# Performance work log

Hardware: AMD Instinct MI355X
Metric: run time of the kernel (lower is better)

## Reference

```python
import jax, jax.numpy as jnp
import numpy as np
from jax import lax

B, T, D, H = 4, 4096, 1024, 8
DK, DV = 1024, 2048          # expand_k=1.0, expand_v=2.0
RANK, MAXL, LOOPD = 16, 8, 128  # lora_rank, max_loops, dim*loop_dim_fraction
THRESH = 0.99
EPS = 1e-6
GK_SCALE = 16.0              # GLA forget-gate temperature


def setup_inputs() -> dict:
    key = jax.random.key(0)
    ks = jax.random.split(key, 16)
    r = lambda i, shape, s=0.02: jax.random.normal(ks[i], shape, jnp.float32) * s
    return {
        "h": jax.random.normal(ks[0], (B, T, D), jnp.float32),
        "e": jax.random.normal(ks[1], (B, T, D), jnp.float32),
        "norm_w": jnp.ones((D,), jnp.float32),
        "out_norm_w": jnp.ones((D,), jnp.float32),
        "Wq": r(2, (D, DK)), "Wk": r(3, (D, DK)), "Wv": r(4, (D, DV)),
        "Wgk": r(5, (D, DK)), "Wg": r(6, (D, DV)), "Wo": r(7, (DV, D)),
        "lora_A": r(8, (MAXL, D, RANK)), "lora_B": r(9, (MAXL, RANK, D)),
        "inj_A": 0.9 * jnp.eye(D, dtype=jnp.float32) + r(10, (D, D)),
        "inj_B": r(11, (D, D)),
        "act_w": r(12, (D,)),
        "act_b": jnp.full((), -2.0, jnp.float32),  # gradual halting
        "loop_table": r(13, (MAXL, LOOPD)),
        "n_loops": 4,
    }


def rmsnorm(x, w):
    return x * lax.rsqrt(jnp.mean(x * x, axis=-1, keepdims=True) + EPS) * w


def gla(x, Wq, Wk, Wv, Wgk, Wg, Wo, num_heads):
    """Gated Linear Attention: data-dependent forget gates, linear-time recurrent scan."""
    b, t, d = x.shape
    dk, dv = Wq.shape[1], Wv.shape[1]
    dkh, dvh = dk // num_heads, dv // num_heads
    q = (x @ Wq).reshape(b, t, num_heads, dkh) * (dkh ** -0.5)
    k = (x @ Wk).reshape(b, t, num_heads, dkh)
    v = (x @ Wv).reshape(b, t, num_heads, dvh)
    # forget gate alpha in (0,1): exp(logsigmoid(gk)/16)
    alpha = jnp.exp(jax.nn.log_sigmoid(x @ Wgk) / GK_SCALE).reshape(b, t, num_heads, dkh)

    def step(S, qkva):  # S: (b, H, dkh, dvh)
        qt, kt, vt, at = qkva
        S = at[..., None] * S + kt[..., None] * vt[..., None, :]
        ot = jnp.einsum('bhk,bhkv->bhv', qt, S)
        return S, ot

    S0 = jnp.zeros((b, num_heads, dkh, dvh), x.dtype)
    xs = (jnp.swapaxes(q, 0, 1), jnp.swapaxes(k, 0, 1),
          jnp.swapaxes(v, 0, 1), jnp.swapaxes(alpha, 0, 1))
    _, o = lax.scan(step, S0, xs)                  # o: (t, b, H, dvh)
    o = jnp.swapaxes(o, 0, 1).reshape(b, t, dv)
    o = o * jax.nn.silu(x @ Wg)                    # output gate
    return o @ Wo


def reference(h, e, norm_w, out_norm_w, Wq, Wk, Wv, Wgk, Wg, Wo,
              lora_A, lora_B, inj_A, inj_B, act_w, act_b, loop_table, n_loops):
    b, t_len, d = h.shape
    halted = jnp.zeros((b, t_len), bool)
    cum = jnp.zeros((b, t_len), h.dtype)
    h_out = jnp.zeros_like(h)
    loopd = loop_table.shape[1]
    for t in range(n_loops):  # small fixed depth loop (structurally distinct LoRA/embed per t)
        # loop index embedding on first loopd channels
        h = h.at[..., :loopd].add(loop_table[t])
        h_norm = rmsnorm(h + e, norm_w)
        g = gla(h_norm, Wq, Wk, Wv, Wgk, Wg, Wo, H)   # dropout: eval mode (identity)
        g = g + (g @ lora_A[t]) @ lora_B[t]            # depth LoRA
        h = h @ inj_A.T + e @ inj_B.T + g              # LTI injection: A.h + B.e + gla
        # ACT halting accumulate
        p = jax.nn.sigmoid(h @ act_w + act_b)          # (b, t_len)
        running = ~halted
        p_eff = jnp.where(running, p, jnp.zeros_like(p))
        new_cum = cum + p_eff
        newly = running & (new_cum >= THRESH)
        w = jnp.where(newly, 1.0 - cum, p_eff)         # remainder for newly-halted
        h_out = h_out + w[..., None] * h
        cum = new_cum
        halted = halted | newly
    return rmsnorm(h_out, out_norm_w)
```

## Files before the change

### kernel.cpp

```cpp
#include <hip/hip_runtime.h>

#define BB 4
#define TT 4096
#define DD 1024
#define HH 8
#define DKK 1024
#define DVV 2048
#define MR (BB*TT)
#define DKH 128
#define DVH 256
#define NLOOPS 4
#define LCH 128
#define NCH (TT/LCH)
#define PADW 136
#define NPROJ 7168

#define WS_NEED 662310912ull

__device__ __attribute__((aligned(256))) unsigned char g_ws[WS_NEED];

typedef __bf16 bf16x8 __attribute__((ext_vector_type(8)));
typedef float  f32x4  __attribute__((ext_vector_type(4)));

__device__ __forceinline__ unsigned short f2bfu(float f) {
    unsigned int u = __builtin_bit_cast(unsigned int, f);
    u += 0x7fffu + ((u >> 16) & 1u);
    return (unsigned short)(u >> 16);
}
__device__ __forceinline__ float bfu2f(unsigned short s) {
    unsigned int u = ((unsigned int)s) << 16;
    return __builtin_bit_cast(float, u);
}

__device__ __forceinline__ void gld_lds16(const void* g, void* l) {
    __builtin_amdgcn_global_load_lds(
        (__attribute__((address_space(1))) void*)const_cast<void*>(g),
        (__attribute__((address_space(3))) void*)l, 16, 0, 0);
}

__global__ __launch_bounds__(256) void k_transpose_bf16(
    const float* __restrict__ in, unsigned short* __restrict__ out, int K, int N)
{
    __shared__ float tile[64][65];
    int k0 = blockIdx.y * 64, n0 = blockIdx.x * 64;
    int tx = threadIdx.x & 63, ty = threadIdx.x >> 6;
    #pragma unroll
    for (int r = 0; r < 64; r += 4)
        tile[ty + r][tx] = in[(size_t)(k0 + ty + r) * N + n0 + tx];
    __syncthreads();
    #pragma unroll
    for (int r = 0; r < 64; r += 4)
        out[(size_t)(n0 + ty + r) * K + k0 + tx] = f2bfu(tile[tx][ty + r]);
}

__global__ __launch_bounds__(256) void k_conv_e(
    const float* __restrict__ e, unsigned short* __restrict__ he)
{
    size_t gid = (size_t)blockIdx.x * 256 + threadIdx.x;
    size_t b4 = gid * 4;
    size_t row = b4 >> 10; int col = (int)(b4 & 1023);
    float4 v = *(const float4*)&e[row * 1024 + col];
    *(ushort4*)&he[row * 2048 + 1024 + col] =
        make_ushort4(f2bfu(v.x), f2bfu(v.y), f2bfu(v.z), f2bfu(v.w));
}

__global__ __launch_bounds__(256) void k_conv_injcomb(
    const float* __restrict__ injA, const float* __restrict__ injB,
    unsigned short* __restrict__ WinjT, float* __restrict__ diag)
{
    int idx = blockIdx.x * 256 + threadIdx.x;
    int i = idx >> 10, j = idx & 1023;
    float va = injA[idx], vb = injB[idx];
    unsigned short ua;
    if (i == j) { diag[i] = va; ua = 0; }
    else        { ua = f2bfu(va); }
    WinjT[(size_t)i * 2048 + j] = ua;
    WinjT[(size_t)i * 2048 + 1024 + j] = f2bfu(vb);
}

__global__ __launch_bounds__(256) void k_prep(
    float* __restrict__ h, const float* __restrict__ e,
    const float* __restrict__ norm_w, const float* __restrict__ ltab,
    unsigned short* __restrict__ he, unsigned short* __restrict__ xn_bf)
{
    int row = blockIdx.x, tid = threadIdx.x;
    size_t base = (size_t)row * DD + tid * 4;
    float4 hv = *(float4*)&h[base];
    if (tid < 32) {
        float4 lv = *(const float4*)&ltab[tid * 4];
        hv.x += lv.x; hv.y += lv.y; hv.z += lv.z; hv.w += lv.w;
        *(float4*)&h[base] = hv;
    }
    float4 ev = *(const float4*)&e[base];
    float sx = hv.x + ev.x, sy = hv.y + ev.y, sz = hv.z + ev.z, sw = hv.w + ev.w;
    float partial = sx*sx + sy*sy + sz*sz + sw*sw;
    __shared__ float red[256];
    red[tid] = partial; __syncthreads();
    for (int st = 128; st > 0; st >>= 1) {
        if (tid < st) red[tid] += red[tid + st];
        __syncthreads();
    }
    float rms = rsqrtf(red[0] * (1.0f / DD) + 1e-6f);
    float4 wv = *(const float4*)&norm_w[tid * 4];
    *(ushort4*)&xn_bf[base] = make_ushort4(
        f2bfu(sx * rms * wv.x), f2bfu(sy * rms * wv.y),
        f2bfu(sz * rms * wv.z), f2bfu(sw * rms * wv.w));
    *(ushort4*)&he[(size_t)row * 2048 + tid * 4] =
        make_ushort4(f2bfu(hv.x), f2bfu(hv.y), f2bfu(hv.z), f2bfu(hv.w));
}

template<int KB>
__device__ __forceinline__ void gemm8_core(
    const char* __restrict__ Ab, const char* __restrict__ Bb,
    int bm, int bn, char* sm, f32x4 (&acc)[8][4])
{
    constexpr int NKT = KB / 128;
    const int tid = threadIdx.x;
    const int lane = tid & 63;
    const int wave = tid >> 6;
    const int wm = wave >> 2, wn = wave & 3;
    const int ln15 = lane & 15, q4 = lane >> 4;
    const int xorv = (ln15 & 7) << 4;
    const int xc0 = (q4 * 16) ^ xorv;
    const int xc1 = (64 + q4 * 16) ^ xorv;

    const int L0 = tid * 16;
    const int L1 = 8192 + tid * 16;
    const int lin0 = L0 ^ (((L0 >> 7) & 7) << 4);
    const int lin1 = L1 ^ (((L1 >> 7) & 7) << 4);
    const int sr0 = lin0 >> 7, sc0 = lin0 & 127;
    const int sr1 = lin1 >> 7, sc1 = lin1 & 127;

    bf16x8 av[4][2];
    bf16x8 bv[2][2][2];

    auto STAGE = [&](const char* gb, int row0, int kcol, int region) {
        gld_lds16(gb + (size_t)(row0 + sr0) * KB + (kcol + sc0), sm + region + L0);
        gld_lds16(gb + (size_t)(row0 + sr1) * KB + (kcol + sc1), sm + region + L1);
    };

#define LD_AV(CB, MH) \
    _Pragma("unroll") \
    for (int i2 = 0; i2 < 4; ++i2) { \
        const char* rp = sm + (CB) + ((MH) * 16384) \
                       + ((wm * 64 + i2 * 16 + ln15) * 128); \
        av[i2][0] = *(const bf16x8*)(rp + xc0); \
        av[i2][1] = *(const bf16x8*)(rp + xc1); \
    }
#define LD_BV(CB, NH) \
    _Pragma("unroll") \
    for (int j2 = 0; j2 < 2; ++j2) { \
        const char* rp = sm + (CB) + 32768 + ((NH) * 16384) \
                       + ((wn * 32 + j2 * 16 + ln15) * 128); \
        bv[NH][j2][0] = *(const bf16x8*)(rp + xc0); \
        bv[NH][j2][1] = *(const bf16x8*)(rp + xc1); \
    }
#define MFMA_Q(MH, NH) \
    __builtin_amdgcn_s_setprio(1); \
    _Pragma("unroll") \
    for (int i2 = 0; i2 < 4; ++i2) \
        _Pragma("unroll") \
        for (int j2 = 0; j2 < 2; ++j2) { \
            acc[(MH)*4+i2][(NH)*2+j2] = __builtin_amdgcn_mfma_f32_16x16x32_bf16( \
                av[i2][0], bv[NH][j2][0], acc[(MH)*4+i2][(NH)*2+j2], 0, 0, 0); \
            acc[(MH)*4+i2][(NH)*2+j2] = __builtin_amdgcn_mfma_f32_16x16x32_bf16( \
                av[i2][1], bv[NH][j2][1], acc[(MH)*4+i2][(NH)*2+j2], 0, 0, 0); \
        } \
    __builtin_amdgcn_s_setprio(0);

    STAGE(Ab, bm,       0, 0);
    STAGE(Bb, bn,       0, 32768);
    STAGE(Bb, bn + 128, 0, 49152);
    STAGE(Ab, bm + 128, 0, 16384);

    #pragma unroll 2
    for (int kt = 0; kt < NKT - 1; ++kt) {
        const int cb = (kt & 1) << 16;
        const int sb = cb ^ 65536;
        const int kcol = (kt + 1) * 128;
        STAGE(Ab, bm, kcol, sb);
        asm volatile("s_waitcnt vmcnt(6)" ::: "memory");
        __builtin_amdgcn_s_barrier();
        LD_AV(cb, 0)
        LD_BV(cb, 0)
        MFMA_Q(0, 0)
        STAGE(Bb, bn, kcol, sb + 32768);
        asm volatile("s_waitcnt vmcnt(6)" ::: "memory");
        __builtin_amdgcn_s_barrier();
        LD_BV(cb, 1)
        MFMA_Q(0, 1)
        STAGE(Bb, bn + 128, kcol, sb + 49152);
        asm volatile("s_waitcnt vmcnt(6)" ::: "memory");
        __builtin_amdgcn_s_barrier();
        LD_AV(cb, 1)
        MFMA_Q(1, 1)
        STAGE(Ab, bm + 128, kcol, sb + 16384);
        MFMA_Q(1, 0)
    }
    {
        const int cb = ((NKT - 1) & 1) << 16;
        asm volatile("s_waitcnt vmcnt(4)" ::: "memory");
        __builtin_amdgcn_s_barrier();
        LD_AV(cb, 0)
        LD_BV(cb, 0)
        MFMA_Q(0, 0)
        asm volatile("s_waitcnt vmcnt(2)" ::: "memory");
        __builtin_amdgcn_s_barrier();
        LD_BV(cb, 1)
        MFMA_Q(0, 1)
        asm volatile("s_waitcnt vmcnt(0)" ::: "memory");
        __builtin_amdgcn_s_barrier();
        LD_AV(cb, 1)
        MFMA_Q(1, 1)
        MFMA_Q(1, 0)
    }
#undef LD_AV
#undef LD_BV
#undef MFMA_Q
}

__global__ __launch_bounds__(512, 2) void k_gemm_proj8(
    const unsigned short* __restrict__ A, const unsigned short* __restrict__ Bt,
    unsigned short* __restrict__ qout, unsigned short* __restrict__ kout,
    float* __restrict__ lgout, unsigned short* __restrict__ vout,
    unsigned short* __restrict__ xgout, float qscale)
{
    extern __shared__ char sm[];
    int bid = blockIdx.x;
    int nb = (bid & 7) * 224 + (bid >> 3);
    int bm = (nb / 28) * 256, bn = (nb % 28) * 256;

    f32x4 acc[8][4];
    #pragma unroll
    for (int i = 0; i < 8; ++i)
        #pragma unroll
        for (int j = 0; j < 4; ++j) { f32x4 z = {0,0,0,0}; acc[i][j] = z; }

    gemm8_core<2048>((const char*)A, (const char*)Bt, bm, bn, sm, acc);

    const int tid = threadIdx.x, lane = tid & 63, wave = tid >> 6;
    const int wm = wave >> 2, wn = wave & 3;
    const int ln15 = lane & 15, q4 = lane >> 4;

    if (bn >= 2048 && bn < 3072) {
        int cb = bn - 2048;
        #pragma unroll
        for (int fm = 0; fm < 8; ++fm) {
            int mh = fm >> 2, i2 = fm & 3;
            int rowb = bm + mh * 128 + wm * 64 + i2 * 16 + q4 * 4;
            #pragma unroll
            for (int fn = 0; fn < 4; ++fn) {
                int nh = fn >> 1, j2 = fn & 1;
                int col = cb + nh * 128 + wn * 32 + j2 * 16 + ln15;
                #pragma unroll
                for (int r = 0; r < 4; ++r) {
                    float v = acc[fm][fn][r];
                    v = (fminf(v, 0.f) - log1pf(expf(-fabsf(v)))) * 0.0625f;
                    lgout[(size_t)(rowb + r) * 1024 + col] = v;
                }
            }
        }
    } else {
        unsigned short* obuf; int stride, cb;
        float scale = 1.f;
        if (bn < 1024)      { obuf = qout;  stride = 1024; cb = bn;        scale = qscale; }
        else if (bn < 2048) { obuf = kout;  stride = 1024; cb = bn - 1024; }
        else if (bn < 5120) { obuf = vout;  stride = 2048; cb = bn - 3072; }
        else                { obuf = xgout; stride = 2048; cb = bn - 5120; }
        #pragma unroll
        for (int fm = 0; fm < 8; ++fm) {
            int mh = fm >> 2, i2 = fm & 3;
            int rowb = bm + mh * 128 + wm * 64 + i2 * 16 + q4 * 4;
            #pragma unroll
            for (int fn = 0; fn < 4; ++fn) {
                int nh = fn >> 1, j2 = fn & 1;
                int col = cb + nh * 128 + wn * 32 + j2 * 16 + ln15;
                #pragma unroll
                for (int r = 0; r < 4; ++r)
                    obuf[(size_t)(rowb + r) * stride + col] =
                        f2bfu(acc[fm][fn][r] * scale);
            }
        }
    }
}

template<int HASADD, int HASDIAG, int KB>
__global__ __launch_bounds__(512, 2) void k_gemm8_f32(
    const unsigned short* __restrict__ A, const unsigned short* __restrict__ Bt,
    float* __restrict__ out, const float* __restrict__ addend,
    const float* __restrict__ hsrc, const float* __restrict__ diag, int N)
{
    extern __shared__ char sm[];
    int bid = blockIdx.x;
    int cpx = gridDim.x >> 3;
    int nb = (bid & 7) * cpx + (bid >> 3);
    int nbn = N >> 8;
    int bm = (nb / nbn) * 256, bn = (nb % nbn) * 256;

    f32x4 acc[8][4];
    #pragma unroll
    for (int i = 0; i < 8; ++i)
        #pragma unroll
        for (int j = 0; j < 4; ++j) { f32x4 z = {0,0,0,0}; acc[i][j] = z; }

    gemm8_core<KB>((const char*)A, (const char*)Bt, bm, bn, sm, acc);

    const int tid = threadIdx.x, lane = tid & 63, wave = tid >> 6;
    const int wm = wave >> 2, wn = wave & 3;
    const int ln15 = lane & 15, q4 = lane >> 4;

    #pragma unroll
    for (int fm = 0; fm < 8; ++fm) {
        int mh = fm >> 2, i2 = fm & 3;
        int rowb = bm + mh * 128 + wm * 64 + i2 * 16 + q4 * 4;
        #pragma unroll
        for (int fn = 0; fn < 4; ++fn) {
            int nh = fn >> 1, j2 = fn & 1;
            int col = bn + nh * 128 + wn * 32 + j2 * 16 + ln15;
            float dg = 0.f;
            if (HASDIAG) dg = diag[col];
            #pragma unroll
            for (int r = 0; r < 4; ++r) {
                size_t oi = (size_t)(rowb + r) * N + col;
                float v = acc[fm][fn][r];
                if (HASDIAG) v += hsrc[oi] * dg;
                if (HASADD)  v += addend[oi];
                out[oi] = v;
            }
        }
    }
}

__global__ __launch_bounds__(256) void k_c1(
    const float* __restrict__ lg, unsigned short* __restrict__ q,
    unsigned short* __restrict__ kk, float* __restrict__ dLe)
{
    int chunk = blockIdx.x;
    int bh = blockIdx.y * 2 + (threadIdx.x >> 7);
    int b = bh >> 3, h = bh & 7;
    int i = threadIdx.x & 127;
    size_t r0 = (size_t)b * TT + (size_t)chunk * LCH;
    float c = 0.f, e = 1.f;
    for (int t = 0; t < LCH; ++t) {
        size_t off = (r0 + t) * DKK + h * DKH + i;
        c += lg[off];
        e = __expf(c);
        float ei = __expf(-c);
        q[off] = f2bfu(bfu2f(q[off]) * e);
        kk[off] = f2bfu(bfu2f(kk[off]) * ei);
    }
    dLe[((size_t)chunk * 32 + bh) * DKH + i] = e;
}

__global__ __launch_bounds__(256, 1) void k_c2(
    const unsigned short* __restrict__ q, const unsigned short* __restrict__ kk,
    const unsigned short* __restrict__ v, unsigned short* __restrict__ ob,
    float* __restrict__ U)
{
    extern __shared__ unsigned short smd[];
    unsigned short* lQ  = smd;
    unsigned short* lK  = smd + LCH * PADW;
    unsigned short* lKT = smd + 2 * LCH * PADW;
    unsigned short* lVT = smd + 3 * LCH * PADW;

    int chunk = blockIdx.x, bh = blockIdx.y;
    int b = bh >> 3, h = bh & 7;
    int tid = threadIdx.x, lane = tid & 63, wave = tid >> 6;
    int wm = wave >> 1, wn = wave & 1;
    int quad = lane >> 4, mr = lane & 15;
    size_t r0 = (size_t)b * TT + (size_t)chunk * LCH;

    #pragma unroll
    for (int ps = 0; ps < 8; ++ps) {
        int idx = ps * 256 + tid;
        int row = idx >> 4, c8 = (idx & 15) * 8;
        size_t g = (r0 + row) * DKK + h * DKH + c8;
        *(int4*)&lQ[row * PADW + c8] = *(const int4*)&q[g];
        union { int4 w; unsigned short u[8]; } tmp;
        tmp.w = *(const int4*)&kk[g];
        *(int4*)&lK[row * PADW + c8] = tmp.w;
        #pragma unroll
        for (int u2 = 0; u2 < 8; ++u2)
            lKT[(c8 + u2) * PADW + row] = tmp.u[u2];
    }
    __syncthreads();

    f32x4 pa[4][4];
    #pragma unroll
    for (int i = 0; i < 4; ++i)
        #pragma unroll
        for (int j = 0; j < 4; ++j) { f32x4 z = {0,0,0,0}; pa[i][j] = z; }
    for (int k0 = 0; k0 < DKH; k0 += 32) {
        bf16x8 av[4], bv[4];
        #pragma unroll
        for (int t2 = 0; t2 < 4; ++t2) {
            av[t2] = *(const bf16x8*)&lQ[(wm * 64 + t2 * 16 + mr) * PADW + k0 + quad * 8];
            bv[t2] = *(const bf16x8*)&lK[(wn * 64 + t2 * 16 + mr) * PADW + k0 + quad * 8];
        }
        #pragma unroll
        for (int tm = 0; tm < 4; ++tm)
            #pragma unroll
            for (int tn = 0; tn < 4; ++tn)
                pa[tm][tn] = __builtin_amdgcn_mfma_f32_16x16x32_bf16(
                    av[tm], bv[tn], pa[tm][tn], 0, 0, 0);
    }
    __syncthreads();

    #pragma unroll
    for (int tm = 0; tm < 4; ++tm)
        #pragma unroll
        for (int tn = 0; tn < 4; ++tn)
            #pragma unroll
            for (int r = 0; r < 4; ++r) {
                int trow = wm * 64 + tm * 16 + quad * 4 + r;
                int scol = wn * 64 + tn * 16 + mr;
                float pv = (trow >= scol) ? pa[tm][tn][r] : 0.f;
                lQ[trow * PADW + scol] = f2bfu(pv);
            }
    #pragma unroll
    for (int ps = 0; ps < 8; ++ps) {
        int idx = ps * 256 + tid;
        int s = idx >> 4, j8 = (idx & 15) * 8;
        size_t g = (r0 + s) * DVV + h * DVH + j8;
        union { int4 w; unsigned short u[8]; } tmp;
        tmp.w = *(const int4*)&v[g];
        #pragma unroll
        for (int u2 = 0; u2 < 8; ++u2)
            lVT[(j8 + u2) * PADW + s] = tmp.u[u2];
    }
    __syncthreads();

    #pragma unroll 1
    for (int panel = 0; panel < 2; ++panel) {
        f32x4 oa[4][4], ua[4][4];
        #pragma unroll
        for (int i = 0; i < 4; ++i)
            #pragma unroll
            for (int j = 0; j < 4; ++j) { f32x4 z = {0,0,0,0}; oa[i][j] = z; ua[i][j] = z; }
        for (int k0 = 0; k0 < LCH; k0 += 32) {
            bf16x8 pv[4], kt[4], vb[4];
            #pragma unroll
            for (int t2 = 0; t2 < 4; ++t2) {
                pv[t2] = *(const bf16x8*)&lQ [(wm * 64 + t2 * 16 + mr) * PADW + k0 + quad * 8];
                kt[t2] = *(const bf16x8*)&lKT[(wm * 64 + t2 * 16 + mr) * PADW + k0 + quad * 8];
                vb[t2] = *(const bf16x8*)&lVT[(wn * 64 + t2 * 16 + mr) * PADW + k0 + quad * 8];
            }
            #pragma unroll
            for (int tm = 0; tm < 4; ++tm)
                #pragma unroll
                for (int tn = 0; tn < 4; ++tn) {
                    oa[tm][tn] = __builtin_amdgcn_mfma_f32_16x16x32_bf16(
                        pv[tm], vb[tn], oa[tm][tn], 0, 0, 0);
                    ua[tm][tn] = __builtin_amdgcn_mfma_f32_16x16x32_bf16(
                        kt[tm], vb[tn], ua[tm][tn], 0, 0, 0);
                }
        }
        #pragma unroll
        for (int tm = 0; tm < 4; ++tm)
            #pragma unroll
            for (int tn = 0; tn < 4; ++tn)
                #pragma unroll
                for (int r = 0; r < 4; ++r) {
                    int m_ = wm * 64 + tm * 16 + quad * 4 + r;
                    int j_ = panel * 128 + wn * 64 + tn * 16 + mr;
                    ob[(r0 + m_) * DVV + h * DVH + j_] = f2bfu(oa[tm][tn][r]);
                    U[(((size_t)chunk * 32 + bh) * DKH + m_) * DVH + j_] = ua[tm][tn][r];
                }
        __syncthreads();
        if (panel == 0) {
            #pragma unroll
            for (int ps = 0; ps < 8; ++ps) {
                int idx = ps * 256 + tid;
                int s = idx >> 4, j8 = (idx & 15) * 8;
                size_t g = (r0 + s) * DVV + h * DVH + 128 + j8;
                union { int4 w; unsigned short u[8]; } tmp;
                tmp.w = *(const int4*)&v[g];
                #pragma unroll
                for (int u2 = 0; u2 < 8; ++u2)
                    lVT[(j8 + u2) * PADW + s] = tmp.u[u2];
            }
            __syncthreads();
        }
    }
}

__global__ __launch_bounds__(256) void k_c3(
    float* __restrict__ U, const float* __restrict__ dLe)
{
    int gid = blockIdx.x * 256 + threadIdx.x;
    int bh = gid >> 13;
    int rem = gid & 8191;
    int i = rem >> 6, j4 = rem & 63;
    float4 S = make_float4(0.f, 0.f, 0.f, 0.f);
    for (int c = 0; c < NCH; ++c) {
        size_t off = (((size_t)c * 32 + bh) * DKH + i) * DVH + j4 * 4;
        float4 u = *(float4*)&U[off];
        *(float4*)&U[off] = S;
        float d = dLe[((size_t)c * 32 + bh) * DKH + i];
        S.x = d * (S.x + u.x); S.y = d * (S.y + u.y);
        S.z = d * (S.z + u.z); S.w = d * (S.w + u.w);
    }
}

__global__ __launch_bounds__(256, 1) void k_c4(
    const unsigned short* __restrict__ q, const float* __restrict__ S,
    unsigned short* __restrict__ ob, const unsigned short* __restrict__ xg)
{
    extern __shared__ unsigned short smd[];
    unsigned short* lQ  = smd;
    unsigned short* lST = smd + LCH * PADW;

    int chunk = blockIdx.x, bh = blockIdx.y;
    int b = bh >> 3, h = bh & 7;
    int tid = threadIdx.x, lane = tid & 63, wave = tid >> 6;
    int wm = wave >> 1, wn = wave & 1;
    int quad = lane >> 4, mr = lane & 15;
    size_t r0 = (size_t)b * TT + (size_t)chunk * LCH;

    #pragma unroll
    for (int ps = 0; ps < 8; ++ps) {
        int idx = ps * 256 + tid;
        int row = idx >> 4, c8 = (idx & 15) * 8;
        size_t g = (r0 + row) * DKK + h * DKH + c8;
        *(int4*)&lQ[row * PADW + c8] = *(const int4*)&q[g];
    }

    #pragma unroll 1
    for (int panel = 0; panel < 2; ++panel) {
        __syncthreads();
        #pragma unroll
        for (int ps = 0; ps < 16; ++ps) {
            int idx = ps * 256 + tid;
            int i = idx >> 5, j4 = idx & 31;
            float4 sv = *(const float4*)&S[(((size_t)chunk * 32 + bh) * DKH + i) * DVH
                                           + panel * 128 + j4 * 4];
            lST[(j4 * 4 + 0) * PADW + i] = f2bfu(sv.x);
            lST[(j4 * 4 + 1) * PADW + i] = f2bfu(sv.y);
            lST[(j4 * 4 + 2) * PADW + i] = f2bfu(sv.z);
            lST[(j4 * 4 + 3) * PADW + i] = f2bfu(sv.w);
        }
        __syncthreads();

        f32x4 oa[4][4];
        #pragma unroll
        for (int i = 0; i < 4; ++i)
            #pragma unroll
            for (int j = 0; j < 4; ++j) { f32x4 z = {0,0,0,0}; oa[i][j] = z; }
        for (int k0 = 0; k0 < DKH; k0 += 32) {
            bf16x8 av[4], bv[4];
            #pragma unroll
            for (int t2 = 0; t2 < 4; ++t2) {
                av[t2] = *(const bf16x8*)&lQ [(wm * 64 + t2 * 16 + mr) * PADW + k0 + quad * 8];
                bv[t2] = *(const bf16x8*)&lST[(wn * 64 + t2 * 16 + mr) * PADW + k0 + quad * 8];
            }
            #pragma unroll
            for (int tm = 0; tm < 4; ++tm)
                #pragma unroll
                for (int tn = 0; tn < 4; ++tn)
                    oa[tm][tn] = __builtin_amdgcn_mfma_f32_16x16x32_bf16(
                        av[tm], bv[tn], oa[tm][tn], 0, 0, 0);
        }
        #pragma unroll
        for (int tm = 0; tm < 4; ++tm)
            #pragma unroll
            for (int tn = 0; tn < 4; ++tn)
                #pragma unroll
                for (int r = 0; r < 4; ++r) {
                    int t_ = wm * 64 + tm * 16 + quad * 4 + r;
                    int j_ = panel * 128 + wn * 64 + tn * 16 + mr;
                    size_t oi = (r0 + t_) * DVV + h * DVH + j_;
                    float ov = bfu2f(ob[oi]) + oa[tm][tn][r];
                    float xf = bfu2f(xg[oi]);
                    ob[oi] = f2bfu(ov * xf / (1.f + expf(-xf)));
                }
    }
}

__global__ __launch_bounds__(256) void k_lora1(
    const float* __restrict__ G, const float* __restrict__ A, float* __restrict__ tmp)
{
    int row = blockIdx.x * 4 + (threadIdx.x >> 6);
    int lane = threadIdx.x & 63;
    float acc[16];
    #pragma unroll
    for (int r = 0; r < 16; ++r) acc[r] = 0.f;
    const float* grow = G + (size_t)row * DD;
    for (int k2 = lane; k2 < DD; k2 += 64) {
        float g = grow[k2];
        const float4* ar = (const float4*)(A + k2 * 16);
        float4 a0 = ar[0], a1 = ar[1], a2 = ar[2], a3 = ar[3];
        acc[0] = fmaf(g, a0.x, acc[0]);  acc[1] = fmaf(g, a0.y, acc[1]);
        acc[2] = fmaf(g, a0.z, acc[2]);  acc[3] = fmaf(g, a0.w, acc[3]);
        acc[4] = fmaf(g, a1.x, acc[4]);  acc[5] = fmaf(g, a1.y, acc[5]);
        acc[6] = fmaf(g, a1.z, acc[6]);  acc[7] = fmaf(g, a1.w, acc[7]);
        acc[8] = fmaf(g, a2.x, acc[8]);  acc[9] = fmaf(g, a2.y, acc[9]);
        acc[10] = fmaf(g, a2.z, acc[10]); acc[11] = fmaf(g, a2.w, acc[11]);
        acc[12] = fmaf(g, a3.x, acc[12]); acc[13] = fmaf(g, a3.y, acc[13]);
        acc[14] = fmaf(g, a3.z, acc[14]); acc[15] = fmaf(g, a3.w, acc[15]);
    }
    #pragma unroll
    for (int off = 32; off >= 1; off >>= 1)
        #pragma unroll
        for (int r = 0; r < 16; ++r) acc[r] += __shfl_xor(acc[r], off);
    if (lane == 0) {
        #pragma unroll
        for (int r = 0; r < 16; ++r) tmp[(size_t)row * 16 + r] = acc[r];
    }
}

__global__ __launch_bounds__(256) void k_lora2(
    float* __restrict__ G, const float* __restrict__ tmp, const float* __restrict__ Bm)
{
    int row = blockIdx.x, tid = threadIdx.x;
    __shared__ float t16[16];
    if (tid < 16) t16[tid] = tmp[(size_t)row * 16 + tid];
    __syncthreads();
    size_t base = (size_t)row * DD + tid * 4;
    float4 acc = *(float4*)&G[base];
    #pragma unroll
    for (int r = 0; r < 16; ++r) {
        float tv = t16[r];
        float4 bv = *(const float4*)&Bm[r * DD + tid * 4];
        acc.x = fmaf(tv, bv.x, acc.x); acc.y = fmaf(tv, bv.y, acc.y);
        acc.z = fmaf(tv, bv.z, acc.z); acc.w = fmaf(tv, bv.w, acc.w);
    }
    *(float4*)&G[base] = acc;
}

__global__ __launch_bounds__(256) void k_act(
    const float* __restrict__ h, const float* __restrict__ act_w,
    const float* __restrict__ act_b, float* __restrict__ out,
    float* __restrict__ cum, int* __restrict__ halted)
{
    int row = blockIdx.x, tid = threadIdx.x;
    size_t base = (size_t)row * DD + tid * 4;
    float4 hv = *(const float4*)&h[base];
    float4 wv = *(const float4*)&act_w[tid * 4];
    float partial = hv.x*wv.x + hv.y*wv.y + hv.z*wv.z + hv.w*wv.w;
    __shared__ float red[256];
    __shared__ float s_cm;
    __shared__ int s_hl;
    if (tid == 0) { s_cm = cum[row]; s_hl = halted[row]; }
    red[tid] = partial; __syncthreads();
    for (int st = 128; st > 0; st >>= 1) {
        if (tid < st) red[tid] += red[tid + st];
        __syncthreads();
    }
    float p = 1.f / (1.f + expf(-(red[0] + act_b[0])));
    float cm = s_cm;
    int hl = s_hl;
    float p_eff = hl ? 0.f : p;
    float ncum = cm + p_eff;
    int newly = (!hl) && (ncum >= 0.99f);
    float w = newly ? (1.f - cm) : p_eff;
    float4 ho = *(float4*)&out[base];
    ho.x += w * hv.x; ho.y += w * hv.y; ho.z += w * hv.z; ho.w += w * hv.w;
    *(float4*)&out[base] = ho;
    if (tid == 0) { cum[row] = ncum; halted[row] = hl | newly; }
}

__global__ __launch_bounds__(256) void k_final(
    float* __restrict__ io, const float* __restrict__ w)
{
    int row = blockIdx.x, tid = threadIdx.x;
    size_t base = (size_t)row * DD + tid * 4;
    float4 hv = *(const float4*)&io[base];
    float partial = hv.x*hv.x + hv.y*hv.y + hv.z*hv.z + hv.w*hv.w;
    __shared__ float red[256];
    red[tid] = partial; __syncthreads();
    for (int st = 128; st > 0; st >>= 1) {
        if (tid < st) red[tid] += red[tid + st];
        __syncthreads();
    }
    float rms = rsqrtf(red[0] * (1.0f / DD) + 1e-6f);
    float4 wv = *(const float4*)&w[tid * 4];
    float4 o = make_float4(hv.x*rms*wv.x, hv.y*rms*wv.y, hv.z*rms*wv.z, hv.w*rms*wv.w);
    *(float4*)&io[base] = o;
}

extern "C" void kernel_launch(void* const* d_in, const int* in_sizes, int n_in,
                              void* d_out, int out_size, void* d_ws, size_t ws_size,
                              hipStream_t stream)
{
    const float* in_h       = (const float*)d_in[0];
    const float* in_e       = (const float*)d_in[1];
    const float* norm_w     = (const float*)d_in[2];
    const float* out_norm_w = (const float*)d_in[3];
    const float* Wq   = (const float*)d_in[4];
    const float* Wk   = (const float*)d_in[5];
    const float* Wv   = (const float*)d_in[6];
    const float* Wgk  = (const float*)d_in[7];
    const float* Wg   = (const float*)d_in[8];
    const float* Wo   = (const float*)d_in[9];
    const float* lora_A = (const float*)d_in[10];
    const float* lora_B = (const float*)d_in[11];
    const float* inj_A  = (const float*)d_in[12];
    const float* inj_B  = (const float*)d_in[13];
    const float* act_w  = (const float*)d_in[14];
    const float* act_b  = (const float*)d_in[15];
    const float* loop_table = (const float*)d_in[16];

    char* p;
    if (ws_size >= WS_NEED) {
        p = (char*)d_ws;
    } else {
        void* sym = nullptr;
        hipGetSymbolAddress(&sym, HIP_SYMBOL(g_ws));
        p = (char*)sym;
    }

    float* h      = (float*)p;            p += (size_t)MR * DD * 4;
    unsigned short* he_bf = (unsigned short*)p; p += (size_t)MR * 2048 * 2;
    unsigned short* xn_bf = (unsigned short*)p; p += (size_t)MR * DD * 2;
    unsigned short* q_bf  = (unsigned short*)p; p += (size_t)MR * DKK * 2;
    unsigned short* k_bf  = (unsigned short*)p; p += (size_t)MR * DKK * 2;
    unsigned short* v_bf  = (unsigned short*)p; p += (size_t)MR * DVV * 2;
    unsigned short* xg_bf = (unsigned short*)p; p += (size_t)MR * DVV * 2;
    float* lgbuf  = (float*)p;            p += (size_t)MR * DKK * 4;
    unsigned short* ob0   = (unsigned short*)p; p += (size_t)MR * DVV * 2;
    float* U      = (float*)p;            p += (size_t)NCH * 32 * DKH * DVH * 4;
    float* dLe    = (float*)p;            p += (size_t)NCH * 32 * DKH * 4;
    unsigned short* WprojT = (unsigned short*)p; p += (size_t)NPROJ * DKK * 2;
    unsigned short* WoT    = (unsigned short*)p; p += (size_t)DD * DVV * 2;
    unsigned short* WinjT  = (unsigned short*)p; p += (size_t)DD * 2048 * 2;
    float* diagA = (float*)p;             p += DD * 4;
    float* tmp16 = (float*)p;             p += (size_t)MR * 16 * 4;
    float* cum   = (float*)p;             p += MR * 4;
    int*   halted = (int*)p;              p += MR * 4;
    float* g2 = lgbuf;
    float* h_out = (float*)d_out;

    hipMemcpyAsync(h, in_h, (size_t)MR * DD * 4, hipMemcpyDeviceToDevice, stream);
    hipMemsetAsync(h_out, 0, (size_t)MR * DD * 4, stream);
    hipMemsetAsync(cum, 0, MR * 4, stream);
    hipMemsetAsync(halted, 0, MR * 4, stream);

    k_transpose_bf16<<<dim3(16, 16), 256, 0, stream>>>(Wq,  WprojT,              DD, DKK);
    k_transpose_bf16<<<dim3(16, 16), 256, 0, stream>>>(Wk,  WprojT + 1024*1024,  DD, DKK);
    k_transpose_bf16<<<dim3(16, 16), 256, 0, stream>>>(Wgk, WprojT + 2048*1024,  DD, DKK);
    k_transpose_bf16<<<dim3(32, 16), 256, 0, stream>>>(Wv,  WprojT + 3072*1024,  DD, DVV);
    k_transpose_bf16<<<dim3(32, 16), 256, 0, stream>>>(Wg,  WprojT + (size_t)5120*1024, DD, DVV);
    k_transpose_bf16<<<dim3(16, 32), 256, 0, stream>>>(Wo,  WoT, DVV, DD);
    k_conv_injcomb<<<4096, 256, 0, stream>>>(inj_A, inj_B, WinjT, diagA);
    k_conv_e<<<MR * DD / 1024, 256, 0, stream>>>(in_e, he_bf);

    const float qscale = 0.08838834764831845f;

    for (int t = 0; t < NLOOPS; ++t) {
        k_prep<<<MR, 256, 0, stream>>>(h, in_e, norm_w, loop_table + t * 128, he_bf, xn_bf);

        k_gemm_proj8<<<1792, 512, 131072, stream>>>(
            xn_bf, WprojT, q_bf, k_bf, lgbuf, v_bf, xg_bf, qscale);

        k_c1<<<dim3(NCH, 16), 256, 0, stream>>>(lgbuf, q_bf, k_bf, dLe);
        k_c2<<<dim3(NCH, 32), 256, 4 * LCH * PADW * 2, stream>>>(
            q_bf, k_bf, v_bf, ob0, U);
        k_c3<<<1024, 256, 0, stream>>>(U, dLe);
        k_c4<<<dim3(NCH, 32), 256, 2 * LCH * PADW * 2, stream>>>(q_bf, U, ob0, xg_bf);

        k_gemm8_f32<0, 0, 4096><<<256, 512, 131072, stream>>>(
            ob0, WoT, g2, nullptr, nullptr, nullptr, DD);

        k_lora1<<<MR / 4, 256, 0, stream>>>(g2, lora_A + (size_t)t * DD * 16, tmp16);
        k_lora2<<<MR, 256, 0, stream>>>(g2, tmp16, lora_B + (size_t)t * 16 * DD);

        k_gemm8_f32<1, 1, 4096><<<256, 512, 131072, stream>>>(
            he_bf, WinjT, h, g2, h, diagA, DD);

        k_act<<<MR, 256, 0, stream>>>(h, act_w, act_b, h_out, cum, halted);
    }

    k_final<<<MR, 256, 0, stream>>>(h_out, out_norm_w);
}
```

Baseline: 4.177 ms.

## Make projection GEMM persistent with cross-tile prefetch and fewer barriers

The projection GEMM now launches 256 persistent blocks, each processing 7 consecutive output tiles. While it computes the last K-step of one tile it preloads the first K-slice of the next, which hides the prologue load latency. The shared gemm core also merges two LDS load phases, dropping one barrier per K-iteration. The risks are a fixed-size 7-tile schedule that may unbalance the work across CUs, the loss of the old blockIdx swizzle for L2 locality, and the epilogue stores no longer overlapping with other blocks.

```diff
diff --git a/kernel.cpp b/kernel.cpp
--- a/kernel.cpp
+++ b/kernel.cpp
@@ -109,36 +109,6 @@
         make_ushort4(f2bfu(hv.x), f2bfu(hv.y), f2bfu(hv.z), f2bfu(hv.w));
 }
 
-template<int KB>
-__device__ __forceinline__ void gemm8_core(
-    const char* __restrict__ Ab, const char* __restrict__ Bb,
-    int bm, int bn, char* sm, f32x4 (&acc)[8][4])
-{
-    constexpr int NKT = KB / 128;
-    const int tid = threadIdx.x;
-    const int lane = tid & 63;
-    const int wave = tid >> 6;
-    const int wm = wave >> 2, wn = wave & 3;
-    const int ln15 = lane & 15, q4 = lane >> 4;
-    const int xorv = (ln15 & 7) << 4;
-    const int xc0 = (q4 * 16) ^ xorv;
-    const int xc1 = (64 + q4 * 16) ^ xorv;
-
-    const int L0 = tid * 16;
-    const int L1 = 8192 + tid * 16;
-    const int lin0 = L0 ^ (((L0 >> 7) & 7) << 4);
-    const int lin1 = L1 ^ (((L1 >> 7) & 7) << 4);
-    const int sr0 = lin0 >> 7, sc0 = lin0 & 127;
-    const int sr1 = lin1 >> 7, sc1 = lin1 & 127;
-
-    bf16x8 av[4][2];
-    bf16x8 bv[2][2][2];
-
-    auto STAGE = [&](const char* gb, int row0, int kcol, int region) {
-        gld_lds16(gb + (size_t)(row0 + sr0) * KB + (kcol + sc0), sm + region + L0);
-        gld_lds16(gb + (size_t)(row0 + sr1) * KB + (kcol + sc1), sm + region + L1);
-    };
-
 #define LD_AV(CB, MH) \
     _Pragma("unroll") \
     for (int i2 = 0; i2 < 4; ++i2) { \
@@ -168,6 +138,36 @@
         } \
     __builtin_amdgcn_s_setprio(0);
 
+template<int KB>
+__device__ __forceinline__ void gemm8_core(
+    const char* __restrict__ Ab, const char* __restrict__ Bb,
+    int bm, int bn, char* sm, f32x4 (&acc)[8][4])
+{
+    constexpr int NKT = KB / 128;
+    const int tid = threadIdx.x;
+    const int lane = tid & 63;
+    const int wave = tid >> 6;
+    const int wm = wave >> 2, wn = wave & 3;
+    const int ln15 = lane & 15, q4 = lane >> 4;
+    const int xorv = (ln15 & 7) << 4;
+    const int xc0 = (q4 * 16) ^ xorv;
+    const int xc1 = (64 + q4 * 16) ^ xorv;
+
+    const int L0 = tid * 16;
+    const int L1 = 8192 + tid * 16;
+    const int lin0 = L0 ^ (((L0 >> 7) & 7) << 4);
+    const int lin1 = L1 ^ (((L1 >> 7) & 7) << 4);
+    const int sr0 = lin0 >> 7, sc0 = lin0 & 127;
+    const int sr1 = lin1 >> 7, sc1 = lin1 & 127;
+
+    bf16x8 av[4][2];
+    bf16x8 bv[2][2][2];
+
+    auto STAGE = [&](const char* gb, int row0, int kcol, int region) {
+        gld_lds16(gb + (size_t)(row0 + sr0) * KB + (kcol + sc0), sm + region + L0);
+        gld_lds16(gb + (size_t)(row0 + sr1) * KB + (kcol + sc1), sm + region + L1);
+    };
+
     STAGE(Ab, bm,       0, 0);
     STAGE(Bb, bn,       0, 32768);
     STAGE(Bb, bn + 128, 0, 49152);
@@ -179,15 +179,13 @@
         const int sb = cb ^ 65536;
         const int kcol = (kt + 1) * 128;
         STAGE(Ab, bm, kcol, sb);
-        asm volatile("s_waitcnt vmcnt(6)" ::: "memory");
+        asm volatile("s_waitcnt vmcnt(4)" ::: "memory");
         __builtin_amdgcn_s_barrier();
         LD_AV(cb, 0)
         LD_BV(cb, 0)
+        LD_BV(cb, 1)
         MFMA_Q(0, 0)
         STAGE(Bb, bn, kcol, sb + 32768);
-        asm volatile("s_waitcnt vmcnt(6)" ::: "memory");
-        __builtin_amdgcn_s_barrier();
-        LD_BV(cb, 1)
         MFMA_Q(0, 1)
         STAGE(Bb, bn + 128, kcol, sb + 49152);
         asm volatile("s_waitcnt vmcnt(6)" ::: "memory");
@@ -199,14 +197,12 @@
     }
     {
         const int cb = ((NKT - 1) & 1) << 16;
-        asm volatile("s_waitcnt vmcnt(4)" ::: "memory");
+        asm volatile("s_waitcnt vmcnt(2)" ::: "memory");
         __builtin_amdgcn_s_barrier();
         LD_AV(cb, 0)
         LD_BV(cb, 0)
+        LD_BV(cb, 1)
         MFMA_Q(0, 0)
-        asm volatile("s_waitcnt vmcnt(2)" ::: "memory");
-        __builtin_amdgcn_s_barrier();
-        LD_BV(cb, 1)
         MFMA_Q(0, 1)
         asm volatile("s_waitcnt vmcnt(0)" ::: "memory");
         __builtin_amdgcn_s_barrier();
@@ -214,73 +210,153 @@
         MFMA_Q(1, 1)
         MFMA_Q(1, 0)
     }
-#undef LD_AV
-#undef LD_BV
-#undef MFMA_Q
-}
-
-__global__ __launch_bounds__(512, 2) void k_gemm_proj8(
+}
+
+__global__ __launch_bounds__(512, 2) void k_gemm_proj8p(
     const unsigned short* __restrict__ A, const unsigned short* __restrict__ Bt,
     unsigned short* __restrict__ qout, unsigned short* __restrict__ kout,
     float* __restrict__ lgout, unsigned short* __restrict__ vout,
     unsigned short* __restrict__ xgout, float qscale)
 {
     extern __shared__ char sm[];
-    int bid = blockIdx.x;
-    int nb = (bid & 7) * 224 + (bid >> 3);
-    int bm = (nb / 28) * 256, bn = (nb % 28) * 256;
-
-    f32x4 acc[8][4];
-    #pragma unroll
-    for (int i = 0; i < 8; ++i)
-        #pragma unroll
-        for (int j = 0; j < 4; ++j) { f32x4 z = {0,0,0,0}; acc[i][j] = z; }
-
-    gemm8_core<2048>((const char*)A, (const char*)Bt, bm, bn, sm, acc);
-
+    constexpr int KB = 2048;
+    const char* Ab = (const char*)A;
+    const char* Bb = (const char*)Bt;
     const int tid = threadIdx.x, lane = tid & 63, wave = tid >> 6;
     const int wm = wave >> 2, wn = wave & 3;
     const int ln15 = lane & 15, q4 = lane >> 4;
-
-    if (bn >= 2048 && bn < 3072) {
-        int cb = bn - 2048;
-        #pragma unroll
-        for (int fm = 0; fm < 8; ++fm) {
-            int mh = fm >> 2, i2 = fm & 3;
-            int rowb = bm + mh * 128 + wm * 64 + i2 * 16 + q4 * 4;
-            #pragma unroll
-            for (int fn = 0; fn < 4; ++fn) {
-                int nh = fn >> 1, j2 = fn & 1;
-                int col = cb + nh * 128 + wn * 32 + j2 * 16 + ln15;
+    const int xorv = (ln15 & 7) << 4;
+    const int xc0 = (q4 * 16) ^ xorv;
+    const int xc1 = (64 + q4 * 16) ^ xorv;
+    const int L0 = tid * 16, L1 = 8192 + tid * 16;
+    const int lin0 = L0 ^ (((L0 >> 7) & 7) << 4);
+    const int lin1 = L1 ^ (((L1 >> 7) & 7) << 4);
+    const int sr0 = lin0 >> 7, sc0 = lin0 & 127;
+    const int sr1 = lin1 >> 7, sc1 = lin1 & 127;
+
+    bf16x8 av[4][2];
+    bf16x8 bv[2][2][2];
+    f32x4 acc[8][4];
+
+    auto STAGE = [&](const char* gb, int row0, int kcol, int region) {
+        gld_lds16(gb + (size_t)(row0 + sr0) * KB + (kcol + sc0), sm + region + L0);
+        gld_lds16(gb + (size_t)(row0 + sr1) * KB + (kcol + sc1), sm + region + L1);
+    };
+
+    int nbC = blockIdx.x * 7;
+    int bmC = (nbC / 28) * 256, bnC = (nbC % 28) * 256;
+
+    STAGE(Ab, bmC, 0, 0);
+    STAGE(Bb, bnC, 0, 32768);
+    STAGE(Bb, bnC + 128, 0, 49152);
+    STAGE(Ab, bmC + 128, 0, 16384);
+
+    #pragma unroll 1
+    for (int tile = 0; tile < 7; ++tile) {
+        const int nbN = nbC + 1;
+        const int bmN = (nbN / 28) * 256, bnN = (nbN % 28) * 256;
+        #pragma unroll
+        for (int i = 0; i < 8; ++i)
+            #pragma unroll
+            for (int j = 0; j < 4; ++j) { f32x4 z = {0,0,0,0}; acc[i][j] = z; }
+
+        #pragma unroll 2
+        for (int kt = 0; kt < 15; ++kt) {
+            const int cb = (kt & 1) << 16;
+            const int sb = cb ^ 65536;
+            const int kcol = (kt + 1) * 128;
+            STAGE(Ab, bmC, kcol, sb);
+            asm volatile("s_waitcnt vmcnt(4)" ::: "memory");
+            __builtin_amdgcn_s_barrier();
+            LD_AV(cb, 0)
+            LD_BV(cb, 0)
+            LD_BV(cb, 1)
+            MFMA_Q(0, 0)
+            STAGE(Bb, bnC, kcol, sb + 32768);
+            MFMA_Q(0, 1)
+            STAGE(Bb, bnC + 128, kcol, sb + 49152);
+            asm volatile("s_waitcnt vmcnt(6)" ::: "memory");
+            __builtin_amdgcn_s_barrier();
+            LD_AV(cb, 1)
+            MFMA_Q(1, 1)
+            STAGE(Ab, bmC + 128, kcol, sb + 16384);
+            MFMA_Q(1, 0)
+        }
+        {
+            const int cb = 65536;
+            if (tile < 6) {
+                STAGE(Ab, bmN, 0, 0);
+                asm volatile("s_waitcnt vmcnt(4)" ::: "memory");
+                __builtin_amdgcn_s_barrier();
+                LD_AV(cb, 0)
+                LD_BV(cb, 0)
+                LD_BV(cb, 1)
+                MFMA_Q(0, 0)
+                STAGE(Bb, bnN, 0, 32768);
+                MFMA_Q(0, 1)
+                STAGE(Bb, bnN + 128, 0, 49152);
+                asm volatile("s_waitcnt vmcnt(6)" ::: "memory");
+                __builtin_amdgcn_s_barrier();
+                LD_AV(cb, 1)
+                MFMA_Q(1, 1)
+                STAGE(Ab, bmN + 128, 0, 16384);
+                MFMA_Q(1, 0)
+            } else {
+                asm volatile("s_waitcnt vmcnt(2)" ::: "memory");
+                __builtin_amdgcn_s_barrier();
+                LD_AV(cb, 0)
+                LD_BV(cb, 0)
+                LD_BV(cb, 1)
+                MFMA_Q(0, 0)
+                MFMA_Q(0, 1)
+                asm volatile("s_waitcnt vmcnt(0)" ::: "memory");
+                __builtin_amdgcn_s_barrier();
+                LD_AV(cb, 1)
+                MFMA_Q(1, 1)
+                MFMA_Q(1, 0)
+            }
+        }
+        if (bnC >= 2048 && bnC < 3072) {
+            int cbc = bnC - 2048;
+            #pragma unroll
+            for (int fm = 0; fm < 8; ++fm) {
+                int mh = fm >> 2, i2 = fm & 3;
+                int rowb = bmC + mh * 128 + wm * 64 + i2 * 16 + q4 * 4;
                 #pragma unroll
-                for (int r = 0; r < 4; ++r) {
-                    float v = acc[fm][fn][r];
-                    v = (fminf(v, 0.f) - log1pf(expf(-fabsf(v)))) * 0.0625f;
-                    lgout[(size_t)(rowb + r) * 1024 + col] = v;
+                for (int fn = 0; fn < 4; ++fn) {
+                    int nh = fn >> 1, j2 = fn & 1;
+                    int col = cbc + nh * 128 + wn * 32 + j2 * 16 + ln15;
+                    #pragma unroll
+                    for (int r = 0; r < 4; ++r) {
+                        float v = acc[fm][fn][r];
+                        v = (fminf(v, 0.f) - log1pf(expf(-fabsf(v)))) * 0.0625f;
+                        lgout[(size_t)(rowb + r) * 1024 + col] = v;
+                    }
+                }
+            }
+        } else {
+            unsigned short* obuf; int stride, cbc;
+            float scale = 1.f;
+            if (bnC < 1024)      { obuf = qout;  stride = 1024; cbc = bnC;        scale = qscale; }
+            else if (bnC < 2048) { obuf = kout;  stride = 1024; cbc = bnC - 1024; }
+            else if (bnC < 5120) { obuf = vout;  stride = 2048; cbc = bnC - 3072; }
+            else                 { obuf = xgout; stride = 2048; cbc = bnC - 5120; }
+            #pragma unroll
+            for (int fm = 0; fm < 8; ++fm) {
+                int mh = fm >> 2, i2 = fm & 3;
+                int rowb = bmC + mh * 128 + wm * 64 + i2 * 16 + q4 * 4;
+                #pragma unroll
+                for (int fn = 0; fn < 4; ++fn) {
+                    int nh = fn >> 1, j2 = fn & 1;
+                    int col = cbc + nh * 128 + wn * 32 + j2 * 16 + ln15;
+                    #pragma unroll
+                    for (int r = 0; r < 4; ++r)
+                        obuf[(size_t)(rowb + r) * stride + col] =
+                            f2bfu(acc[fm][fn][r] * scale);
                 }
             }
         }
-    } else {
-        unsigned short* obuf; int stride, cb;
-        float scale = 1.f;
-        if (bn < 1024)      { obuf = qout;  stride = 1024; cb = bn;        scale = qscale; }
-        else if (bn < 2048) { obuf = kout;  stride = 1024; cb = bn - 1024; }
-        else if (bn < 5120) { obuf = vout;  stride = 2048; cb = bn - 3072; }
-        else                { obuf = xgout; stride = 2048; cb = bn - 5120; }
-        #pragma unroll
-        for (int fm = 0; fm < 8; ++fm) {
-            int mh = fm >> 2, i2 = fm & 3;
-            int rowb = bm + mh * 128 + wm * 64 + i2 * 16 + q4 * 4;
-            #pragma unroll
-            for (int fn = 0; fn < 4; ++fn) {
-                int nh = fn >> 1, j2 = fn & 1;
-                int col = cb + nh * 128 + wn * 32 + j2 * 16 + ln15;
-                #pragma unroll
-                for (int r = 0; r < 4; ++r)
-                    obuf[(size_t)(rowb + r) * stride + col] =
-                        f2bfu(acc[fm][fn][r] * scale);
-            }
-        }
+        nbC = nbN; bmC = bmN; bnC = bnN;
     }
 }
 
@@ -330,6 +406,10 @@
         }
     }
 }
+
+#undef LD_AV
+#undef LD_BV
+#undef MFMA_Q
 
 __global__ __launch_bounds__(256) void k_c1(
     const float* __restrict__ lg, unsigned short* __restrict__ q,
@@ -391,18 +471,18 @@
         #pragma unroll
         for (int j = 0; j < 4; ++j) { f32x4 z = {0,0,0,0}; pa[i][j] = z; }
     for (int k0 = 0; k0 < DKH; k0 += 32) {
-        bf16x8 av[4], bv[4];
+        bf16x8 av[4], bvv[4];
         #pragma unroll
         for (int t2 = 0; t2 < 4; ++t2) {
             av[t2] = *(const bf16x8*)&lQ[(wm * 64 + t2 * 16 + mr) * PADW + k0 + quad * 8];
-            bv[t2] = *(const bf16x8*)&lK[(wn * 64 + t2 * 16 + mr) * PADW + k0 + quad * 8];
+            bvv[t2] = *(const bf16x8*)&lK[(wn * 64 + t2 * 16 + mr) * PADW + k0 + quad * 8];
         }
         #pragma unroll
         for (int tm = 0; tm < 4; ++tm)
             #pragma unroll
             for (int tn = 0; tn < 4; ++tn)
                 pa[tm][tn] = __builtin_amdgcn_mfma_f32_16x16x32_bf16(
-                    av[tm], bv[tn], pa[tm][tn], 0, 0, 0);
+                    av[tm], bvv[tn], pa[tm][tn], 0, 0, 0);
     }
     __syncthreads();
 
@@ -547,18 +627,18 @@
             #pragma unroll
             for (int j = 0; j < 4; ++j) { f32x4 z = {0,0,0,0}; oa[i][j] = z; }
         for (int k0 = 0; k0 < DKH; k0 += 32) {
-            bf16x8 av[4], bv[4];
+            bf16x8 av[4], bvv[4];
             #pragma unroll
             for (int t2 = 0; t2 < 4; ++t2) {
                 av[t2] = *(const bf16x8*)&lQ [(wm * 64 + t2 * 16 + mr) * PADW + k0 + quad * 8];
-                bv[t2] = *(const bf16x8*)&lST[(wn * 64 + t2 * 16 + mr) * PADW + k0 + quad * 8];
+                bvv[t2] = *(const bf16x8*)&lST[(wn * 64 + t2 * 16 + mr) * PADW + k0 + quad * 8];
             }
             #pragma unroll
             for (int tm = 0; tm < 4; ++tm)
                 #pragma unroll
                 for (int tn = 0; tn < 4; ++tn)
                     oa[tm][tn] = __builtin_amdgcn_mfma_f32_16x16x32_bf16(
-                        av[tm], bv[tn], oa[tm][tn], 0, 0, 0);
+                        av[tm], bvv[tn], oa[tm][tn], 0, 0, 0);
         }
         #pragma unroll
         for (int tm = 0; tm < 4; ++tm)
@@ -749,7 +829,7 @@
     for (int t = 0; t < NLOOPS; ++t) {
         k_prep<<<MR, 256, 0, stream>>>(h, in_e, norm_w, loop_table + t * 128, he_bf, xn_bf);
 
-        k_gemm_proj8<<<1792, 512, 131072, stream>>>(
+        k_gemm_proj8p<<<256, 512, 131072, stream>>>(
             xn_bf, WprojT, q_bf, k_bf, lgbuf, v_bf, xg_bf, qscale);
 
         k_c1<<<dim3(NCH, 16), 256, 0, stream>>>(lgbuf, q_bf, k_bf, dLe);
```

Result: slower. 5.192 ms (+24.3%).
